# Performance work log

Measured on AMD Instinct MI355X. Metric: run time of the kernel, lower is better.

Reference implementation:

```python
import jax, jax.numpy as jnp
import numpy as np

N, E, IN_DIM, OUT_DIM = 20000, 320000, 256, 128
EPS = 1e-5  # PyG LayerNorm default eps


def seg_sum(data, idx, n):
    return jax.ops.segment_sum(data, idx, num_segments=n)


def gcn_conv(x, src, dst, emask, W, b, n):
    # GCNConv(improved=True): add self-loops with weight 2, symmetric deg^-1/2 norm.
    # Masked (dropped) edges contribute weight 0 to both degree and aggregation.
    xW = x @ W                               # [n, C_out]
    w = emask.astype(x.dtype)                # [E]
    deg = seg_sum(w, dst, n) + 2.0           # in-degree + self-loop weight 2
    dinv = jax.lax.rsqrt(deg)                # deg >= 2 always
    norm = dinv[src] * w * dinv[dst]         # [E]
    out = seg_sum(xW[src] * norm[:, None], dst, n)
    out = out + (2.0 / deg)[:, None] * xW    # self-loop term: dinv_i * 2 * dinv_i
    return out + b


def graph_norm(x, w, b):
    # PyG LayerNorm(mode='graph'), batch=None: scalar mean/std over ALL entries,
    # then per-channel affine.
    xc = x - x.mean()
    std = jnp.sqrt(jnp.mean(xc * xc))
    return xc / (std + EPS) * w + b


def sag_pool(x, src, dst, emask, wrel, brel, wroot, n, k):
    # SAGPooling: score from GraphConv(in,1) = lin_rel(sum_{j->i} x_j) + lin_root(x_i).
    # lin_rel commutes with the sum, so project to scalar first (cheaper).
    w = emask.astype(x.dtype)
    s_rel = (x @ wrel)[:, 0]                                  # [n]
    score = seg_sum(s_rel[src] * w, dst, n) + brel[0] + (x @ wroot)[:, 0]
    topv, perm = jax.lax.top_k(score, k)                      # ratio=0.5 -> k nodes
    xk = x[perm] * jnp.tanh(topv)[:, None]                    # nonlinearity=tanh
    kept = jnp.zeros((n,), bool).at[perm].set(True)
    inv = jnp.zeros((n,), src.dtype).at[perm].set(jnp.arange(k, dtype=src.dtype))
    new_mask = emask & kept[src] & kept[dst]                  # filter_adj, fixed-size + mask
    return xk, inv[src], inv[dst], new_mask


def setup_inputs() -> dict:
    key = jax.random.key(0)
    ks = jax.random.split(key, 20)
    f = jnp.float32
    inp = {
        "x": jax.random.normal(ks[0], (N, IN_DIM), f),
        "edge_index": jax.random.randint(ks[1], (2, E), 0, N, dtype=jnp.int32),
        "W1": jax.random.normal(ks[2], (IN_DIM, 512), f) * (1.0 / np.sqrt(IN_DIM)),
        "b1": jnp.zeros((512,), f),
        "ln1_w": jnp.ones((512,), f),
        "ln1_b": jnp.zeros((512,), f),
        "p1_wrel": jax.random.normal(ks[3], (512, 1), f) * (1.0 / np.sqrt(512)),
        "p1_brel": jnp.zeros((1,), f),
        "p1_wroot": jax.random.normal(ks[4], (512, 1), f) * (1.0 / np.sqrt(512)),
        "W2": jax.random.normal(ks[5], (512, 256), f) * (1.0 / np.sqrt(512)),
        "b2": jnp.zeros((256,), f),
        "ln2_w": jnp.ones((256,), f),
        "ln2_b": jnp.zeros((256,), f),
        "p2_wrel": jax.random.normal(ks[6], (256, 1), f) * (1.0 / np.sqrt(256)),
        "p2_brel": jnp.zeros((1,), f),
        "p2_wroot": jax.random.normal(ks[7], (256, 1), f) * (1.0 / np.sqrt(256)),
        "Wf": jax.random.normal(ks[8], (256, OUT_DIM), f) * (1.0 / np.sqrt(256)),
        "bf": jnp.zeros((OUT_DIM,), f),
    }
    return inp


def reference(x, edge_index, W1, b1, ln1_w, ln1_b, p1_wrel, p1_brel, p1_wroot,
              W2, b2, ln2_w, ln2_b, p2_wrel, p2_brel, p2_wroot, Wf, bf):
    src, dst = edge_index[0], edge_index[1]
    emask = jnp.ones((E,), bool)
    k1 = (N + 1) // 2   # ceil(0.5 * N)
    k2 = (k1 + 1) // 2

    h = gcn_conv(x, src, dst, emask, W1, b1, N)
    h = jax.nn.relu(graph_norm(h, ln1_w, ln1_b))
    h, src, dst, emask = sag_pool(h, src, dst, emask, p1_wrel, p1_brel, p1_wroot, N, k1)

    h = gcn_conv(h, src, dst, emask, W2, b2, k1)
    h = jax.nn.relu(graph_norm(h, ln2_w, ln2_b))
    h, src, dst, emask = sag_pool(h, src, dst, emask, p2_wrel, p2_brel, p2_wroot, k1, k2)

    g = h.mean(axis=0, keepdims=True)   # global_mean_pool, batch=None -> [1, 256]
    return g @ Wf + bf
```

## Files before the change

kernel.cpp:

```cpp
#include <hip/hip_runtime.h>
#include <math.h>

#define N1 20000
#define NE 320000
#define CIN 256
#define C1 512
#define C2 256
#define K1 10000
#define K2 5000
#define NOUT 128
#define EPSV 1e-5f
#define CM_ROWS 128

typedef __attribute__((ext_vector_type(8))) short bf16x8;
typedef __attribute__((ext_vector_type(4))) float f32x4;

static inline unsigned cdiv(unsigned a, unsigned b) { return (a + b - 1) / b; }

__device__ inline ushort f2bf(float f) {
    unsigned u = __float_as_uint(f);
    unsigned r = u + 0x7FFFu + ((u >> 16) & 1u);
    return (ushort)(r >> 16);
}
__device__ inline float bf2f(ushort u) { return __uint_as_float(((unsigned)u) << 16); }

__global__ void fill_i32(int* __restrict__ p, int v, int n) {
    int i = blockIdx.x * blockDim.x + threadIdx.x;
    if (i < n) p[i] = v;
}

__global__ void f32_to_bf16(const float* __restrict__ in, ushort* __restrict__ out, int n4) {
    int i = blockIdx.x * blockDim.x + threadIdx.x;
    if (i >= n4) return;
    float4 v = reinterpret_cast<const float4*>(in)[i];
    ushort4 o;
    o.x = f2bf(v.x); o.y = f2bf(v.y); o.z = f2bf(v.z); o.w = f2bf(v.w);
    reinterpret_cast<ushort4*>(out)[i] = o;
}

__global__ void conv_transpose_bf16(const float* __restrict__ W, ushort* __restrict__ Wt,
                                    int K, int N) {
    int i = blockIdx.x * blockDim.x + threadIdx.x;
    if (i >= K * N) return;
    int k = i / N, n = i % N;
    Wt[(size_t)n * K + k] = f2bf(W[i]);
}

template <bool BF16OUT, bool STATS>
__global__ __launch_bounds__(256)
void gemm_bf16_mfma(const ushort* __restrict__ A, const ushort* __restrict__ Bt,
                    const float* __restrict__ bias, float* __restrict__ C,
                    ushort* __restrict__ Cb, float* __restrict__ Sp, int M, int N, int K) {
    constexpr int BM = 128, BN = 128, BK = 32;
    constexpr int LDK = BK + 8;
    __shared__ ushort As[BM * LDK];
    __shared__ ushort Bs[BN * LDK];
    int tid = threadIdx.x;
    int wid = tid >> 6, lane = tid & 63;
    int wr = wid >> 1, wc = wid & 1;
    int bm = blockIdx.x * BM, bn = blockIdx.y * BN;
    int lg = lane >> 4, lm = lane & 15;
    f32x4 zero = {0.f, 0.f, 0.f, 0.f};
    f32x4 acc[4][4];
#pragma unroll
    for (int m = 0; m < 4; ++m)
#pragma unroll
        for (int n = 0; n < 4; ++n) acc[m][n] = zero;

    for (int k0 = 0; k0 < K; k0 += BK) {
#pragma unroll
        for (int it = 0; it < 2; ++it) {
            int task = tid * 2 + it;
            int row = task >> 2, c8 = (task & 3) * 8;
            int gm = bm + row;
            bf16x8 v = {0, 0, 0, 0, 0, 0, 0, 0};
            if (gm < M) v = *(const bf16x8*)&A[(size_t)gm * K + k0 + c8];
            *(bf16x8*)&As[row * LDK + c8] = v;
            int gn = bn + row;
            bf16x8 w = {0, 0, 0, 0, 0, 0, 0, 0};
            if (gn < N) w = *(const bf16x8*)&Bt[(size_t)gn * K + k0 + c8];
            *(bf16x8*)&Bs[row * LDK + c8] = w;
        }
        __syncthreads();
        bf16x8 af[4], bfr[4];
#pragma unroll
        for (int m = 0; m < 4; ++m)
            af[m] = *(bf16x8*)&As[(wr * 64 + m * 16 + lm) * LDK + lg * 8];
#pragma unroll
        for (int n = 0; n < 4; ++n)
            bfr[n] = *(bf16x8*)&Bs[(wc * 64 + n * 16 + lm) * LDK + lg * 8];
#pragma unroll
        for (int m = 0; m < 4; ++m)
#pragma unroll
            for (int n = 0; n < 4; ++n)
                acc[m][n] = __builtin_amdgcn_mfma_f32_16x16x32_bf16(af[m], bfr[n], acc[m][n], 0, 0, 0);
        __syncthreads();
    }
    float ls = 0.f, lq = 0.f;
#pragma unroll
    for (int m = 0; m < 4; ++m) {
#pragma unroll
        for (int n = 0; n < 4; ++n) {
            int col = bn + wc * 64 + n * 16 + lm;
            float bv = bias ? bias[col] : 0.f;
#pragma unroll
            for (int r = 0; r < 4; ++r) {
                int row = bm + wr * 64 + m * 16 + lg * 4 + r;
                if (row < M) {
                    float val = acc[m][n][r] + bv;
                    if (BF16OUT) Cb[(size_t)row * N + col] = f2bf(val);
                    else         C[(size_t)row * N + col] = val;
                    if (STATS) { ls += val; lq += val * val; }
                }
            }
        }
    }
    if (STATS) {
        __shared__ float rs[256], rq[256];
        rs[tid] = ls; rq[tid] = lq;
        __syncthreads();
        for (int off = 128; off > 0; off >>= 1) {
            if (tid < off) { rs[tid] += rs[tid + off]; rq[tid] += rq[tid + off]; }
            __syncthreads();
        }
        if (tid == 0) {
            int b = blockIdx.y * gridDim.x + blockIdx.x;
            Sp[2 * b] = rs[0];
            Sp[2 * b + 1] = rq[0];
        }
    }
}

__global__ void count_deg(const int* __restrict__ dst, const int* __restrict__ mask, int E,
                          int* __restrict__ cnt) {
    int e = blockIdx.x * blockDim.x + threadIdx.x;
    if (e >= E) return;
    if (mask && !mask[e]) return;
    atomicAdd(&cnt[dst[e]], 1);
}

__global__ void dp_partial(const int* __restrict__ cnt, int n, int* __restrict__ part) {
    int base = blockIdx.x * 1024 + (int)threadIdx.x * 4;
    int s = 0;
#pragma unroll
    for (int t = 0; t < 4; ++t) {
        int i = base + t;
        if (i < n) s += cnt[i];
    }
    for (int off = 32; off > 0; off >>= 1) s += __shfl_down(s, off);
    __shared__ int sg[4];
    int wid = threadIdx.x >> 6;
    if ((threadIdx.x & 63) == 0) sg[wid] = s;
    __syncthreads();
    if (threadIdx.x == 0) part[blockIdx.x] = sg[0] + sg[1] + sg[2] + sg[3];
}

__global__ void scan64k(int nb, int* __restrict__ part, int* __restrict__ row_n) {
    int lane = threadIdx.x;
    int v0 = (lane < nb) ? part[lane] : 0;
    int v = v0;
    for (int off = 1; off < 64; off <<= 1) {
        int vv = __shfl_up(v, off);
        if (lane >= off) v += vv;
    }
    if (lane == nb - 1) row_n[0] = v;
    if (lane < nb) part[lane] = v - v0;
}

__global__ void dp_final(const int* __restrict__ cnt, int n, const int* __restrict__ part,
                         int* __restrict__ rowstart, int* __restrict__ cursor,
                         float* __restrict__ deg, float* __restrict__ dinv) {
    int base = blockIdx.x * 1024 + (int)threadIdx.x * 4;
    int c[4];
    int s = 0;
#pragma unroll
    for (int t = 0; t < 4; ++t) {
        int i = base + t;
        c[t] = (i < n) ? cnt[i] : 0;
        s += c[t];
    }
    int lane = threadIdx.x & 63, wid = threadIdx.x >> 6;
    int si = s;
    for (int off = 1; off < 64; off <<= 1) {
        int vv = __shfl_up(si, off);
        if (lane >= off) si += vv;
    }
    __shared__ int wg[4];
    if (lane == 63) wg[wid] = si;
    __syncthreads();
    int woff = 0;
    for (int w = 0; w < wid; ++w) woff += wg[w];
    int excl = part[blockIdx.x] + (si - s) + woff;
#pragma unroll
    for (int t = 0; t < 4; ++t) {
        int i = base + t;
        if (i < n) {
            rowstart[i] = excl;
            cursor[i] = excl;
            float dg = (float)c[t] + 2.0f;
            deg[i] = dg;
            dinv[i] = rsqrtf(dg);
        }
        excl += c[t];
    }
}

__global__ void csr_scatter(const int* __restrict__ src, const int* __restrict__ dst,
                            const int* __restrict__ mask, int E,
                            int* __restrict__ cursor, int* __restrict__ csr_src) {
    int e = blockIdx.x * blockDim.x + threadIdx.x;
    if (e >= E) return;
    if (mask && !mask[e]) return;
    int pos = atomicAdd(&cursor[dst[e]], 1);
    csr_src[pos] = src[e];
}

__global__ void aggregate_xb(const int* __restrict__ rowstart, const int* __restrict__ csr_src,
                             const float* __restrict__ deg, const float* __restrict__ dinv,
                             const ushort* __restrict__ xb, ushort* __restrict__ out, int n) {
    int node = blockIdx.x * (blockDim.x >> 6) + ((int)threadIdx.x >> 6);
    if (node >= n) return;
    int lane = threadIdx.x & 63;
    int beg = rowstart[node], end = rowstart[node + 1];
    float di = dinv[node];
    float4 acc = make_float4(0.f, 0.f, 0.f, 0.f);
    int j = beg;
    for (; j + 8 <= end; j += 8) {
        int s[8];
#pragma unroll
        for (int u = 0; u < 8; ++u) s[u] = csr_src[j + u];
        float c[8];
#pragma unroll
        for (int u = 0; u < 8; ++u) c[u] = dinv[s[u]] * di;
        ushort4 t[8];
#pragma unroll
        for (int u = 0; u < 8; ++u)
            t[u] = reinterpret_cast<const ushort4*>(&xb[(size_t)s[u] * CIN])[lane];
#pragma unroll
        for (int u = 0; u < 8; ++u) {
            acc.x += c[u] * bf2f(t[u].x);
            acc.y += c[u] * bf2f(t[u].y);
            acc.z += c[u] * bf2f(t[u].z);
            acc.w += c[u] * bf2f(t[u].w);
        }
    }
    for (; j < end; ++j) {
        int s = csr_src[j];
        float coef = dinv[s] * di;
        ushort4 t = reinterpret_cast<const ushort4*>(&xb[(size_t)s * CIN])[lane];
        acc.x += coef * bf2f(t.x);
        acc.y += coef * bf2f(t.y);
        acc.z += coef * bf2f(t.z);
        acc.w += coef * bf2f(t.w);
    }
    float self = 2.0f / deg[node];
    ushort4 t = reinterpret_cast<const ushort4*>(&xb[(size_t)node * CIN])[lane];
    acc.x += self * bf2f(t.x);
    acc.y += self * bf2f(t.y);
    acc.z += self * bf2f(t.z);
    acc.w += self * bf2f(t.w);
    ushort4 o;
    o.x = f2bf(acc.x); o.y = f2bf(acc.y); o.z = f2bf(acc.z); o.w = f2bf(acc.w);
    reinterpret_cast<ushort4*>(&out[(size_t)node * CIN])[lane] = o;
}

__global__ void aggregate_csr_bf(const int* __restrict__ rowstart, const int* __restrict__ csr_src,
                                 const float* __restrict__ deg, const float* __restrict__ dinv,
                                 const ushort* __restrict__ xWb, const float* __restrict__ b,
                                 float* __restrict__ out, float* __restrict__ Sp, int n) {
    int node = blockIdx.x * (blockDim.x >> 6) + ((int)threadIdx.x >> 6);
    bool valid = node < n;
    int lane = threadIdx.x & 63;
    float ls = 0.f, lq = 0.f;
    if (valid) {
        int beg = rowstart[node], end = rowstart[node + 1];
        float di = dinv[node];
        float4 acc = make_float4(0.f, 0.f, 0.f, 0.f);
        int j = beg;
        for (; j + 8 <= end; j += 8) {
            int s[8];
#pragma unroll
            for (int u = 0; u < 8; ++u) s[u] = csr_src[j + u];
            float c[8];
#pragma unroll
            for (int u = 0; u < 8; ++u) c[u] = dinv[s[u]] * di;
            ushort4 t[8];
#pragma unroll
            for (int u = 0; u < 8; ++u)
                t[u] = reinterpret_cast<const ushort4*>(&xWb[(size_t)s[u] * C2])[lane];
#pragma unroll
            for (int u = 0; u < 8; ++u) {
                acc.x += c[u] * bf2f(t[u].x);
                acc.y += c[u] * bf2f(t[u].y);
                acc.z += c[u] * bf2f(t[u].z);
                acc.w += c[u] * bf2f(t[u].w);
            }
        }
        for (; j < end; ++j) {
            int s = csr_src[j];
            float coef = dinv[s] * di;
            ushort4 t = reinterpret_cast<const ushort4*>(&xWb[(size_t)s * C2])[lane];
            acc.x += coef * bf2f(t.x);
            acc.y += coef * bf2f(t.y);
            acc.z += coef * bf2f(t.z);
            acc.w += coef * bf2f(t.w);
        }
        float self = 2.0f / deg[node];
        ushort4 t = reinterpret_cast<const ushort4*>(&xWb[(size_t)node * C2])[lane];
        float4 bb = reinterpret_cast<const float4*>(b)[lane];
        float4 o;
        o.x = acc.x + self * bf2f(t.x) + bb.x;
        o.y = acc.y + self * bf2f(t.y) + bb.y;
        o.z = acc.z + self * bf2f(t.z) + bb.z;
        o.w = acc.w + self * bf2f(t.w) + bb.w;
        reinterpret_cast<float4*>(&out[(size_t)node * C2])[lane] = o;
        ls = o.x + o.y + o.z + o.w;
        lq = o.x * o.x + o.y * o.y + o.z * o.z + o.w * o.w;
    }
    __shared__ float rs[256], rq[256];
    rs[threadIdx.x] = ls; rq[threadIdx.x] = lq;
    __syncthreads();
    for (int off = 128; off > 0; off >>= 1) {
        if ((int)threadIdx.x < off) {
            rs[threadIdx.x] += rs[threadIdx.x + off];
            rq[threadIdx.x] += rq[threadIdx.x + off];
        }
        __syncthreads();
    }
    if (threadIdx.x == 0) {
        Sp[2 * blockIdx.x] = rs[0];
        Sp[2 * blockIdx.x + 1] = rq[0];
    }
}

__global__ void reduce_final(const float* __restrict__ Sp, int nb, float* __restrict__ S) {
    float s = 0.f, q = 0.f;
    for (int i = threadIdx.x; i < nb; i += 256) {
        s += Sp[2 * i];
        q += Sp[2 * i + 1];
    }
    __shared__ float ls[256], lq[256];
    ls[threadIdx.x] = s; lq[threadIdx.x] = q;
    __syncthreads();
    for (int off = 128; off > 0; off >>= 1) {
        if ((int)threadIdx.x < off) {
            ls[threadIdx.x] += ls[threadIdx.x + off];
            lq[threadIdx.x] += lq[threadIdx.x + off];
        }
        __syncthreads();
    }
    if (threadIdx.x == 0) { S[0] = ls[0]; S[1] = lq[0]; }
}

template <int C>
__global__ void norm_scores(const float* __restrict__ h, int n, const float* __restrict__ S,
                            float inv_cnt, const float* __restrict__ lnw,
                            const float* __restrict__ lnb, const float* __restrict__ wrel,
                            const float* __restrict__ brel, const float* __restrict__ wroot,
                            float* __restrict__ r, float* __restrict__ score) {
    int node = blockIdx.x * (blockDim.x >> 6) + ((int)threadIdx.x >> 6);
    if (node >= n) return;
    int lane = threadIdx.x & 63;
    float mean = S[0] * inv_cnt;
    float var = S[1] * inv_cnt - mean * mean;
    float istd = 1.f / (sqrtf(fmaxf(var, 0.f)) + EPSV);
    const float4* row = reinterpret_cast<const float4*>(&h[(size_t)node * C]);
    float sr = 0.f, st = 0.f;
#pragma unroll
    for (int kk = 0; kk < C / 256; ++kk) {
        int idx = lane + 64 * kk;
        float4 v = row[idx];
        float4 w = reinterpret_cast<const float4*>(lnw)[idx];
        float4 bb = reinterpret_cast<const float4*>(lnb)[idx];
        float4 w4 = reinterpret_cast<const float4*>(wrel)[idx];
        float4 o4 = reinterpret_cast<const float4*>(wroot)[idx];
        v.x = fmaxf((v.x - mean) * istd * w.x + bb.x, 0.f);
        v.y = fmaxf((v.y - mean) * istd * w.y + bb.y, 0.f);
        v.z = fmaxf((v.z - mean) * istd * w.z + bb.z, 0.f);
        v.w = fmaxf((v.w - mean) * istd * w.w + bb.w, 0.f);
        sr += v.x * w4.x + v.y * w4.y + v.z * w4.z + v.w * w4.w;
        st += v.x * o4.x + v.y * o4.y + v.z * o4.z + v.w * o4.w;
    }
    for (int off = 32; off > 0; off >>= 1) {
        sr += __shfl_down(sr, off);
        st += __shfl_down(st, off);
    }
    if (lane == 0) {
        r[node] = sr;
        score[node] = st + brel[0];
    }
}

__global__ void gather_score_key(const int* __restrict__ rowstart, const int* __restrict__ csr_src,
                                 const float* __restrict__ r, float* __restrict__ score,
                                 unsigned* __restrict__ key, int n) {
    int i = blockIdx.x * blockDim.x + threadIdx.x;
    if (i >= n) return;
    float s = score[i];
    int beg = rowstart[i], end = rowstart[i + 1];
    int j = beg;
    for (; j + 4 <= end; j += 4) {
        int s0 = csr_src[j], s1 = csr_src[j + 1], s2 = csr_src[j + 2], s3 = csr_src[j + 3];
        s += r[s0] + r[s1] + r[s2] + r[s3];
    }
    for (; j < end; ++j) s += r[csr_src[j]];
    score[i] = s;
    unsigned u = __float_as_uint(s);
    key[i] = (u & 0x80000000u) ? ~u : (u | 0x80000000u);
}

__global__ void select_thresh_reg(const unsigned* __restrict__ key, int n, unsigned k,
                                  unsigned* __restrict__ sel) {
    __shared__ unsigned hist[256];
    __shared__ unsigned wsum[16];
    __shared__ unsigned s_pref, s_rem;
    int t = threadIdx.x;
    int lane = t & 63, w = t >> 6;

    unsigned kv[20];
#pragma unroll
    for (int i = 0; i < 20; ++i) {
        int idx = t + 1024 * i;
        kv[i] = (idx < n) ? key[idx] : 0u;
    }

    if (t < 256) hist[t] = 0u;
    if (t == 0) { s_pref = 0u; s_rem = k; }
    __syncthreads();

    unsigned pref = 0u, msk = 0u, rem = k;
#pragma unroll
    for (int pass = 0; pass < 4; ++pass) {
        int shift = 24 - 8 * pass;
#pragma unroll
        for (int i = 0; i < 20; ++i) {
            int idx = t + 1024 * i;
            if (idx < n && (kv[i] & msk) == pref)
                atomicAdd(&hist[(kv[i] >> shift) & 255u], 1u);
        }
        __syncthreads();
        unsigned val = (t < 256) ? hist[255 - t] : 0u;
        unsigned si = val;
#pragma unroll
        for (int off = 1; off < 64; off <<= 1) {
            unsigned vv = __shfl_up(si, off);
            if (lane >= off) si += vv;
        }
        if (lane == 63 && w < 4) wsum[w] = si;
        __syncthreads();
        if (t < 256) hist[t] = 0u;
        if (t < 256) {
            unsigned wpre = 0u;
            for (int i = 0; i < w; ++i) wpre += wsum[i];
            unsigned incl = wpre + si;
            unsigned excl = incl - val;
            if (excl < rem && rem <= incl) {
                s_pref = pref | ((unsigned)(255 - t) << shift);
                s_rem = rem - excl;
            }
        }
        __syncthreads();
        pref = s_pref;
        rem = s_rem;
        msk = 0xFFFFFFFFu << shift;
    }
    if (t == 0) { sel[0] = pref; sel[1] = rem; }
}

__global__ void sc_partial(const unsigned* __restrict__ key, int n, const unsigned* __restrict__ sel,
                           int* __restrict__ gpart, int* __restrict__ epart) {
    unsigned thr = sel[0];
    int base = blockIdx.x * 1024 + (int)threadIdx.x * 4;
    int gs = 0, es = 0;
#pragma unroll
    for (int t = 0; t < 4; ++t) {
        int i = base + t;
        if (i < n) {
            unsigned u = key[i];
            gs += (u > thr); es += (u == thr);
        }
    }
    for (int off = 32; off > 0; off >>= 1) {
        gs += __shfl_down(gs, off);
        es += __shfl_down(es, off);
    }
    __shared__ int sg[4], se[4];
    int wid = threadIdx.x >> 6;
    if ((threadIdx.x & 63) == 0) { sg[wid] = gs; se[wid] = es; }
    __syncthreads();
    if (threadIdx.x == 0) {
        gpart[blockIdx.x] = sg[0] + sg[1] + sg[2] + sg[3];
        epart[blockIdx.x] = se[0] + se[1] + se[2] + se[3];
    }
}

__global__ void sc_final(const unsigned* __restrict__ key, int n, const unsigned* __restrict__ sel,
                         const int* __restrict__ gpart, const int* __restrict__ epart,
                         int* __restrict__ kept, int* __restrict__ inv) {
    unsigned thr = sel[0];
    int tie = (int)sel[1];
    int gp0 = 0, ep0 = 0;
    for (int b = 0; b < (int)blockIdx.x; ++b) { gp0 += gpart[b]; ep0 += epart[b]; }
    int base = blockIdx.x * 1024 + (int)threadIdx.x * 4;
    int gl[4], el[4];
    int gs = 0, es = 0;
#pragma unroll
    for (int t = 0; t < 4; ++t) {
        int i = base + t;
        gl[t] = 0; el[t] = 0;
        if (i < n) {
            unsigned u = key[i];
            gl[t] = (u > thr); el[t] = (u == thr);
        }
        gs += gl[t]; es += el[t];
    }
    int lane = threadIdx.x & 63, wid = threadIdx.x >> 6;
    int gi = gs, ei = es;
    for (int off = 1; off < 64; off <<= 1) {
        int gg = __shfl_up(gi, off), ee = __shfl_up(ei, off);
        if (lane >= off) { gi += gg; ei += ee; }
    }
    __shared__ int wg[4], we[4];
    if (lane == 63) { wg[wid] = gi; we[wid] = ei; }
    __syncthreads();
    int wgo = 0, weo = 0;
    for (int w = 0; w < wid; ++w) { wgo += wg[w]; weo += we[w]; }
    int gp = gp0 + (gi - gs) + wgo;
    int ep = ep0 + (ei - es) + weo;
#pragma unroll
    for (int t = 0; t < 4; ++t) {
        int i = base + t;
        if (i < n) {
            int keep = gl[t] | (el[t] & ((ep < tie) ? 1 : 0));
            kept[i] = keep;
            inv[i] = gp + ((ep < tie) ? ep : tie);
        }
        gp += gl[t]; ep += el[t];
    }
}

__global__ void pool_apply_rows(const float* __restrict__ h, const float* __restrict__ score,
                                const int* __restrict__ kept, const int* __restrict__ inv,
                                int n, const float* __restrict__ S, float inv_cnt,
                                const float* __restrict__ lnw, const float* __restrict__ lnb,
                                ushort* __restrict__ hp) {
    int node = blockIdx.x * (blockDim.x >> 6) + ((int)threadIdx.x >> 6);
    if (node >= n) return;
    if (!kept[node]) return;
    int lane = threadIdx.x & 63;
    float mean = S[0] * inv_cnt;
    float var = S[1] * inv_cnt - mean * mean;
    float istd = 1.f / (sqrtf(fmaxf(var, 0.f)) + EPSV);
    float tw = tanhf(score[node]);
    const float4* src = reinterpret_cast<const float4*>(&h[(size_t)node * C1]);
    ushort4* dst = reinterpret_cast<ushort4*>(&hp[(size_t)inv[node] * C1]);
#pragma unroll
    for (int v = 0; v < 2; ++v) {
        int idx = lane + 64 * v;
        float4 a = src[idx];
        float4 w = reinterpret_cast<const float4*>(lnw)[idx];
        float4 bb = reinterpret_cast<const float4*>(lnb)[idx];
        ushort4 o;
        o.x = f2bf(fmaxf((a.x - mean) * istd * w.x + bb.x, 0.f) * tw);
        o.y = f2bf(fmaxf((a.y - mean) * istd * w.y + bb.y, 0.f) * tw);
        o.z = f2bf(fmaxf((a.z - mean) * istd * w.z + bb.z, 0.f) * tw);
        o.w = f2bf(fmaxf((a.w - mean) * istd * w.w + bb.w, 0.f) * tw);
        dst[idx] = o;
    }
}

__global__ void edge_relabel(const int* __restrict__ src, const int* __restrict__ dst, int E,
                             const int* __restrict__ kept, const int* __restrict__ inv,
                             int* __restrict__ src2, int* __restrict__ dst2,
                             int* __restrict__ mask2) {
    int e = blockIdx.x * blockDim.x + threadIdx.x;
    if (e >= E) return;
    int s = src[e], d = dst[e];
    int m = kept[s] & kept[d];
    mask2[e] = m;
    src2[e] = m ? inv[s] : 0;
    dst2[e] = m ? inv[d] : 0;
}

__global__ void colmean_part(const float* __restrict__ h, const float* __restrict__ score,
                             const int* __restrict__ kept, int n, const float* __restrict__ S,
                             float inv_cnt, const float* __restrict__ lnw,
                             const float* __restrict__ lnb, float* __restrict__ Gp) {
    __shared__ float w[CM_ROWS];
    int i0 = blockIdx.x * CM_ROWS;
    int t = threadIdx.x;
    float mean = S[0] * inv_cnt;
    float var = S[1] * inv_cnt - mean * mean;
    float istd = 1.f / (sqrtf(fmaxf(var, 0.f)) + EPSV);
    float wn = lnw[t] * istd;
    float bn = lnb[t] - mean * wn;
    for (int i = t; i < CM_ROWS; i += 256) {
        int idx = i0 + i;
        w[i] = (idx < n && kept[idx]) ? tanhf(score[idx]) : 0.f;
    }
    __syncthreads();
    float acc = 0.f;
    int rows = min(CM_ROWS, n - i0);
#pragma unroll 8
    for (int ri = 0; ri < rows; ++ri)
        acc = fmaf(w[ri], fmaxf(fmaf(h[(size_t)(i0 + ri) * C2 + t], wn, bn), 0.f), acc);
    Gp[blockIdx.x * 256 + t] = acc;
}

__global__ void colmean_final(const float* __restrict__ Gp, int nb, float invk,
                              float* __restrict__ g) {
    int t = threadIdx.x;
    float s = 0.f;
    for (int b = 0; b < nb; ++b) s += Gp[b * 256 + t];
    g[t] = s * invk;
}

__global__ void final_gemv(const float* __restrict__ g, const float* __restrict__ Wf,
                           const float* __restrict__ bf, float* __restrict__ out) {
    int j = threadIdx.x;
    float s = bf[j];
    for (int c = 0; c < 256; ++c) s += g[c] * Wf[c * NOUT + j];
    out[j] = s;
}

extern "C" void kernel_launch(void* const* d_in, const int* in_sizes, int n_in,
                              void* d_out, int out_size, void* d_ws, size_t ws_size,
                              hipStream_t stream) {
    const float* x      = (const float*)d_in[0];
    const int*   ei     = (const int*)d_in[1];
    const float* W1     = (const float*)d_in[2];
    const float* b1     = (const float*)d_in[3];
    const float* ln1w   = (const float*)d_in[4];
    const float* ln1b   = (const float*)d_in[5];
    const float* p1wrel = (const float*)d_in[6];
    const float* p1brel = (const float*)d_in[7];
    const float* p1wroot= (const float*)d_in[8];
    const float* W2     = (const float*)d_in[9];
    const float* b2     = (const float*)d_in[10];
    const float* ln2w   = (const float*)d_in[11];
    const float* ln2b   = (const float*)d_in[12];
    const float* p2wrel = (const float*)d_in[13];
    const float* p2brel = (const float*)d_in[14];
    const float* p2wroot= (const float*)d_in[15];
    const float* Wf     = (const float*)d_in[16];
    const float* bf     = (const float*)d_in[17];
    float* out = (float*)d_out;
    char* ws = (char*)d_ws;

    const int* src1 = ei;
    const int* dst1 = ei + NE;

    const size_t o0     = 0;
    const size_t o1     = 40960000;
    const size_t oXb    = 51200000;
    const size_t oW1t   = 61440000;
    const size_t oW2t   = 61702144;
    const size_t oSrc2  = 61964288;
    const size_t oDst2  = 63244288;
    const size_t oMask2 = 64524288;
    const size_t oCsr   = 65804288;
    const size_t oRow   = 67084288;
    const size_t oCur   = 67164352;
    const size_t oDeg   = 67244352;
    const size_t oDinv  = 67324352;
    const size_t oR     = 67404352;
    const size_t oScore1= 67484352;
    const size_t oKeyu  = 67564352;
    const size_t oKept  = 67644352;
    const size_t oInv   = 67724352;
    const size_t oScore2= 67804352;
    const size_t oKeyu2 = 67844352;
    const size_t oKept2 = 67884352;
    const size_t oInv2  = 67924352;
    const size_t oS     = 67964352;
    const size_t oSel   = 67964416;
    const size_t oGpart = 67964480;
    const size_t oEpart = 67964736;
    const size_t oG     = 67964992;
    const size_t oGp    = 68232256;
    const size_t oSp    = 68314176;

    float*  h1    = (float*)(ws + o0);
    float*  h2    = (float*)(ws + o0);
    ushort* xW2b  = (ushort*)(ws + o0 + 10240000);
    ushort* aggb  = (ushort*)(ws + o1);
    ushort* h1pb  = (ushort*)(ws + o1);
    ushort* xb    = (ushort*)(ws + oXb);
    ushort* W1t   = (ushort*)(ws + oW1t);
    ushort* W2t   = (ushort*)(ws + oW2t);
    int*    src2  = (int*)(ws + oSrc2);
    int*    dst2  = (int*)(ws + oDst2);
    int*    mask2 = (int*)(ws + oMask2);
    int*    csr   = (int*)(ws + oCsr);
    int*    row   = (int*)(ws + oRow);
    int*    cur   = (int*)(ws + oCur);
    float*  deg   = (float*)(ws + oDeg);
    float*  dinv  = (float*)(ws + oDinv);
    float*  r     = (float*)(ws + oR);
    float*  score1= (float*)(ws + oScore1);
    unsigned* keyu  = (unsigned*)(ws + oKeyu);
    int*    kept  = (int*)(ws + oKept);
    int*    inv   = (int*)(ws + oInv);
    float*  score2= (float*)(ws + oScore2);
    unsigned* keyu2 = (unsigned*)(ws + oKeyu2);
    int*    kept2 = (int*)(ws + oKept2);
    int*    inv2  = (int*)(ws + oInv2);
    float*  S     = (float*)(ws + oS);
    unsigned* sel  = (unsigned*)(ws + oSel);
    int*    gpart = (int*)(ws + oGpart);
    int*    epart = (int*)(ws + oEpart);
    float*  g     = (float*)(ws + oG);
    float*  Gp    = (float*)(ws + oGp);
    float*  Sp    = (float*)(ws + oSp);

    const int nb1 = cdiv(N1, 1024);
    const int nb2 = cdiv(K1, 1024);
    const int nbc = cdiv(K1, CM_ROWS);
    const int g1x = cdiv(N1, 128), g1y = C1 / 128;
    const int agg2b = cdiv(K1, 4);

    f32_to_bf16<<<cdiv(N1 * CIN / 4, 256), 256, 0, stream>>>(x, xb, N1 * CIN / 4);

    fill_i32<<<cdiv(N1, 256), 256, 0, stream>>>(cur, 0, N1);
    count_deg<<<cdiv(NE, 256), 256, 0, stream>>>(dst1, nullptr, NE, cur);
    dp_partial<<<nb1, 256, 0, stream>>>(cur, N1, gpart);
    scan64k<<<1, 64, 0, stream>>>(nb1, gpart, row + N1);
    dp_final<<<nb1, 256, 0, stream>>>(cur, N1, gpart, row, cur, deg, dinv);
    csr_scatter<<<cdiv(NE, 256), 256, 0, stream>>>(src1, dst1, nullptr, NE, cur, csr);

    aggregate_xb<<<cdiv(N1, 4), 256, 0, stream>>>(row, csr, deg, dinv, xb, aggb, N1);

    conv_transpose_bf16<<<cdiv(CIN * C1, 256), 256, 0, stream>>>(W1, W1t, CIN, C1);
    gemm_bf16_mfma<false, true><<<dim3(g1x, g1y), 256, 0, stream>>>(
        aggb, W1t, b1, h1, nullptr, Sp, N1, C1, CIN);
    reduce_final<<<1, 256, 0, stream>>>(Sp, g1x * g1y, S);

    norm_scores<C1><<<cdiv(N1, 4), 256, 0, stream>>>(h1, N1, S, 1.f / ((float)N1 * C1),
                                                     ln1w, ln1b, p1wrel, p1brel, p1wroot, r, score1);
    gather_score_key<<<cdiv(N1, 256), 256, 0, stream>>>(row, csr, r, score1, keyu, N1);

    select_thresh_reg<<<1, 1024, 0, stream>>>(keyu, N1, K1, sel);
    sc_partial<<<nb1, 256, 0, stream>>>(keyu, N1, sel, gpart, epart);
    sc_final<<<nb1, 256, 0, stream>>>(keyu, N1, sel, gpart, epart, kept, inv);

    pool_apply_rows<<<cdiv(N1, 4), 256, 0, stream>>>(h1, score1, kept, inv, N1, S,
                                                     1.f / ((float)N1 * C1), ln1w, ln1b, h1pb);
    edge_relabel<<<cdiv(NE, 256), 256, 0, stream>>>(src1, dst1, NE, kept, inv, src2, dst2, mask2);

    conv_transpose_bf16<<<cdiv(C1 * C2, 256), 256, 0, stream>>>(W2, W2t, C1, C2);
    gemm_bf16_mfma<true, false><<<dim3(cdiv(K1, 128), C2 / 128), 256, 0, stream>>>(
        h1pb, W2t, nullptr, nullptr, xW2b, nullptr, K1, C2, C1);

    fill_i32<<<cdiv(K1, 256), 256, 0, stream>>>(cur, 0, K1);
    count_deg<<<cdiv(NE, 256), 256, 0, stream>>>(dst2, mask2, NE, cur);
    dp_partial<<<nb2, 256, 0, stream>>>(cur, K1, gpart);
    scan64k<<<1, 64, 0, stream>>>(nb2, gpart, row + K1);
    dp_final<<<nb2, 256, 0, stream>>>(cur, K1, gpart, row, cur, deg, dinv);
    csr_scatter<<<cdiv(NE, 256), 256, 0, stream>>>(src2, dst2, mask2, NE, cur, csr);

    aggregate_csr_bf<<<agg2b, 256, 0, stream>>>(row, csr, deg, dinv, xW2b, b2, h2, Sp, K1);
    reduce_final<<<1, 256, 0, stream>>>(Sp, agg2b, S);

    norm_scores<C2><<<cdiv(K1, 4), 256, 0, stream>>>(h2, K1, S, 1.f / ((float)K1 * C2),
                                                     ln2w, ln2b, p2wrel, p2brel, p2wroot, r, score2);
    gather_score_key<<<cdiv(K1, 256), 256, 0, stream>>>(row, csr, r, score2, keyu2, K1);

    select_thresh_reg<<<1, 1024, 0, stream>>>(keyu2, K1, K2, sel);
    sc_partial<<<nb2, 256, 0, stream>>>(keyu2, K1, sel, gpart, epart);
    sc_final<<<nb2, 256, 0, stream>>>(keyu2, K1, sel, gpart, epart, kept2, inv2);

    colmean_part<<<nbc, 256, 0, stream>>>(h2, score2, kept2, K1, S, 1.f / ((float)K1 * C2),
                                          ln2w, ln2b, Gp);
    colmean_final<<<1, 256, 0, stream>>>(Gp, nbc, 1.f / (float)K2, g);
    final_gemv<<<1, NOUT, 0, stream>>>(g, Wf, bf, out);
}
```

Baseline: 297.9 us.

## Collapse multi-kernel scans, top-k selection and reductions into fewer launches

```diff
diff --git a/kernel.cpp b/kernel.cpp
--- a/kernel.cpp
+++ b/kernel.cpp
@@ -11,6 +11,7 @@
 #define NOUT 128
 #define EPSV 1e-5f
 #define CM_ROWS 128
+#define KPT 20
 
 typedef __attribute__((ext_vector_type(8))) short bf16x8;
 typedef __attribute__((ext_vector_type(4))) float f32x4;
@@ -24,13 +25,29 @@
 }
 __device__ inline float bf2f(ushort u) { return __uint_as_float(((unsigned)u) << 16); }
 
-__global__ void fill_i32(int* __restrict__ p, int v, int n) {
+__device__ void block_stats(const float* __restrict__ Sp, int nb, float inv_cnt,
+                            float& mean, float& istd) {
+    __shared__ float bs_ls[256], bs_lq[256];
+    float s = 0.f, q = 0.f;
+    for (int i = threadIdx.x; i < nb; i += 256) { s += Sp[2 * i]; q += Sp[2 * i + 1]; }
+    bs_ls[threadIdx.x] = s; bs_lq[threadIdx.x] = q;
+    __syncthreads();
+    for (int off = 128; off > 0; off >>= 1) {
+        if ((int)threadIdx.x < off) {
+            bs_ls[threadIdx.x] += bs_ls[threadIdx.x + off];
+            bs_lq[threadIdx.x] += bs_lq[threadIdx.x + off];
+        }
+        __syncthreads();
+    }
+    mean = bs_ls[0] * inv_cnt;
+    float var = bs_lq[0] * inv_cnt - mean * mean;
+    istd = 1.f / (sqrtf(fmaxf(var, 0.f)) + EPSV);
+}
+
+__global__ void f32_to_bf16(const float* __restrict__ in, ushort* __restrict__ out, int n4,
+                            int* __restrict__ zbuf, int nz) {
     int i = blockIdx.x * blockDim.x + threadIdx.x;
-    if (i < n) p[i] = v;
-}
-
-__global__ void f32_to_bf16(const float* __restrict__ in, ushort* __restrict__ out, int n4) {
-    int i = blockIdx.x * blockDim.x + threadIdx.x;
+    if (i < nz) zbuf[i] = 0;
     if (i >= n4) return;
     float4 v = reinterpret_cast<const float4*>(in)[i];
     ushort4 o;
@@ -139,70 +156,46 @@
     atomicAdd(&cnt[dst[e]], 1);
 }
 
-__global__ void dp_partial(const int* __restrict__ cnt, int n, int* __restrict__ part) {
-    int base = blockIdx.x * 1024 + (int)threadIdx.x * 4;
+__global__ void scan_all(const int* __restrict__ cnt, int n, int* __restrict__ rowstart,
+                         int* __restrict__ cursor, float* __restrict__ deg,
+                         float* __restrict__ dinv) {
+    int t = threadIdx.x;
+    int lane = t & 63, w = t >> 6;
+    int base = t * KPT;
+    int c[KPT];
     int s = 0;
 #pragma unroll
-    for (int t = 0; t < 4; ++t) {
-        int i = base + t;
-        if (i < n) s += cnt[i];
-    }
-    for (int off = 32; off > 0; off >>= 1) s += __shfl_down(s, off);
-    __shared__ int sg[4];
-    int wid = threadIdx.x >> 6;
-    if ((threadIdx.x & 63) == 0) sg[wid] = s;
-    __syncthreads();
-    if (threadIdx.x == 0) part[blockIdx.x] = sg[0] + sg[1] + sg[2] + sg[3];
-}
-
-__global__ void scan64k(int nb, int* __restrict__ part, int* __restrict__ row_n) {
-    int lane = threadIdx.x;
-    int v0 = (lane < nb) ? part[lane] : 0;
-    int v = v0;
-    for (int off = 1; off < 64; off <<= 1) {
-        int vv = __shfl_up(v, off);
-        if (lane >= off) v += vv;
-    }
-    if (lane == nb - 1) row_n[0] = v;
-    if (lane < nb) part[lane] = v - v0;
-}
-
-__global__ void dp_final(const int* __restrict__ cnt, int n, const int* __restrict__ part,
-                         int* __restrict__ rowstart, int* __restrict__ cursor,
-                         float* __restrict__ deg, float* __restrict__ dinv) {
-    int base = blockIdx.x * 1024 + (int)threadIdx.x * 4;
-    int c[4];
-    int s = 0;
-#pragma unroll
-    for (int t = 0; t < 4; ++t) {
-        int i = base + t;
-        c[t] = (i < n) ? cnt[i] : 0;
-        s += c[t];
-    }
-    int lane = threadIdx.x & 63, wid = threadIdx.x >> 6;
+    for (int i = 0; i < KPT; ++i) {
+        int idx = base + i;
+        c[i] = (idx < n) ? cnt[idx] : 0;
+        s += c[i];
+    }
     int si = s;
     for (int off = 1; off < 64; off <<= 1) {
         int vv = __shfl_up(si, off);
         if (lane >= off) si += vv;
     }
-    __shared__ int wg[4];
-    if (lane == 63) wg[wid] = si;
+    __shared__ int wsum[16];
+    if (lane == 63) wsum[w] = si;
     __syncthreads();
-    int woff = 0;
-    for (int w = 0; w < wid; ++w) woff += wg[w];
-    int excl = part[blockIdx.x] + (si - s) + woff;
-#pragma unroll
-    for (int t = 0; t < 4; ++t) {
-        int i = base + t;
-        if (i < n) {
-            rowstart[i] = excl;
-            cursor[i] = excl;
-            float dg = (float)c[t] + 2.0f;
-            deg[i] = dg;
-            dinv[i] = rsqrtf(dg);
-        }
-        excl += c[t];
-    }
+    int wpre = 0;
+    for (int i = 0; i < w; ++i) wpre += wsum[i];
+    int total = 0;
+    for (int i = 0; i < 16; ++i) total += wsum[i];
+    int excl = wpre + si - s;
+#pragma unroll
+    for (int i = 0; i < KPT; ++i) {
+        int idx = base + i;
+        if (idx < n) {
+            rowstart[idx] = excl;
+            cursor[idx] = excl;
+            float dg = (float)c[i] + 2.0f;
+            deg[idx] = dg;
+            dinv[idx] = rsqrtf(dg);
+        }
+        excl += c[i];
+    }
+    if (t == 0) rowstart[n] = total;
 }
 
 __global__ void csr_scatter(const int* __restrict__ src, const int* __restrict__ dst,
@@ -333,37 +326,17 @@
     }
 }
 
-__global__ void reduce_final(const float* __restrict__ Sp, int nb, float* __restrict__ S) {
-    float s = 0.f, q = 0.f;
-    for (int i = threadIdx.x; i < nb; i += 256) {
-        s += Sp[2 * i];
-        q += Sp[2 * i + 1];
-    }
-    __shared__ float ls[256], lq[256];
-    ls[threadIdx.x] = s; lq[threadIdx.x] = q;
-    __syncthreads();
-    for (int off = 128; off > 0; off >>= 1) {
-        if ((int)threadIdx.x < off) {
-            ls[threadIdx.x] += ls[threadIdx.x + off];
-            lq[threadIdx.x] += lq[threadIdx.x + off];
-        }
-        __syncthreads();
-    }
-    if (threadIdx.x == 0) { S[0] = ls[0]; S[1] = lq[0]; }
-}
-
 template <int C>
-__global__ void norm_scores(const float* __restrict__ h, int n, const float* __restrict__ S,
-                            float inv_cnt, const float* __restrict__ lnw,
+__global__ void norm_scores(const float* __restrict__ h, int n, const float* __restrict__ Sp,
+                            int nb, float inv_cnt, const float* __restrict__ lnw,
                             const float* __restrict__ lnb, const float* __restrict__ wrel,
                             const float* __restrict__ brel, const float* __restrict__ wroot,
                             float* __restrict__ r, float* __restrict__ score) {
+    float mean, istd;
+    block_stats(Sp, nb, inv_cnt, mean, istd);
     int node = blockIdx.x * (blockDim.x >> 6) + ((int)threadIdx.x >> 6);
     if (node >= n) return;
     int lane = threadIdx.x & 63;
-    float mean = S[0] * inv_cnt;
-    float var = S[1] * inv_cnt - mean * mean;
-    float istd = 1.f / (sqrtf(fmaxf(var, 0.f)) + EPSV);
     const float4* row = reinterpret_cast<const float4*>(&h[(size_t)node * C]);
     float sr = 0.f, st = 0.f;
 #pragma unroll
@@ -409,46 +382,44 @@
     key[i] = (u & 0x80000000u) ? ~u : (u | 0x80000000u);
 }
 
-__global__ void select_thresh_reg(const unsigned* __restrict__ key, int n, unsigned k,
-                                  unsigned* __restrict__ sel) {
+__global__ void topk_all(const unsigned* __restrict__ key, int n, unsigned k,
+                         int* __restrict__ kept, int* __restrict__ inv) {
     __shared__ unsigned hist[256];
     __shared__ unsigned wsum[16];
     __shared__ unsigned s_pref, s_rem;
+    __shared__ int wgs[16], wes[16];
     int t = threadIdx.x;
     int lane = t & 63, w = t >> 6;
-
-    unsigned kv[20];
-#pragma unroll
-    for (int i = 0; i < 20; ++i) {
-        int idx = t + 1024 * i;
+    int base = t * KPT;
+
+    unsigned kv[KPT];
+#pragma unroll
+    for (int i = 0; i < KPT; ++i) {
+        int idx = base + i;
         kv[i] = (idx < n) ? key[idx] : 0u;
     }
-
     if (t < 256) hist[t] = 0u;
     if (t == 0) { s_pref = 0u; s_rem = k; }
     __syncthreads();
 
     unsigned pref = 0u, msk = 0u, rem = k;
-#pragma unroll
     for (int pass = 0; pass < 4; ++pass) {
         int shift = 24 - 8 * pass;
 #pragma unroll
-        for (int i = 0; i < 20; ++i) {
-            int idx = t + 1024 * i;
+        for (int i = 0; i < KPT; ++i) {
+            int idx = base + i;
             if (idx < n && (kv[i] & msk) == pref)
                 atomicAdd(&hist[(kv[i] >> shift) & 255u], 1u);
         }
         __syncthreads();
         unsigned val = (t < 256) ? hist[255 - t] : 0u;
         unsigned si = val;
-#pragma unroll
         for (int off = 1; off < 64; off <<= 1) {
             unsigned vv = __shfl_up(si, off);
             if (lane >= off) si += vv;
         }
         if (lane == 63 && w < 4) wsum[w] = si;
         __syncthreads();
-        if (t < 256) hist[t] = 0u;
         if (t < 256) {
             unsigned wpre = 0u;
             for (int i = 0; i < w; ++i) wpre += wsum[i];
@@ -459,98 +430,61 @@
                 s_rem = rem - excl;
             }
         }
+        if (t < 256) hist[t] = 0u;
         __syncthreads();
         pref = s_pref;
         rem = s_rem;
         msk = 0xFFFFFFFFu << shift;
     }
-    if (t == 0) { sel[0] = pref; sel[1] = rem; }
-}
-
-__global__ void sc_partial(const unsigned* __restrict__ key, int n, const unsigned* __restrict__ sel,
-                           int* __restrict__ gpart, int* __restrict__ epart) {
-    unsigned thr = sel[0];
-    int base = blockIdx.x * 1024 + (int)threadIdx.x * 4;
+    unsigned thr = pref;
+    int tie = (int)rem;
+
+    int gl[KPT], el[KPT];
     int gs = 0, es = 0;
 #pragma unroll
-    for (int t = 0; t < 4; ++t) {
-        int i = base + t;
-        if (i < n) {
-            unsigned u = key[i];
-            gs += (u > thr); es += (u == thr);
-        }
-    }
-    for (int off = 32; off > 0; off >>= 1) {
-        gs += __shfl_down(gs, off);
-        es += __shfl_down(es, off);
-    }
-    __shared__ int sg[4], se[4];
-    int wid = threadIdx.x >> 6;
-    if ((threadIdx.x & 63) == 0) { sg[wid] = gs; se[wid] = es; }
-    __syncthreads();
-    if (threadIdx.x == 0) {
-        gpart[blockIdx.x] = sg[0] + sg[1] + sg[2] + sg[3];
-        epart[blockIdx.x] = se[0] + se[1] + se[2] + se[3];
-    }
-}
-
-__global__ void sc_final(const unsigned* __restrict__ key, int n, const unsigned* __restrict__ sel,
-                         const int* __restrict__ gpart, const int* __restrict__ epart,
-                         int* __restrict__ kept, int* __restrict__ inv) {
-    unsigned thr = sel[0];
-    int tie = (int)sel[1];
-    int gp0 = 0, ep0 = 0;
-    for (int b = 0; b < (int)blockIdx.x; ++b) { gp0 += gpart[b]; ep0 += epart[b]; }
-    int base = blockIdx.x * 1024 + (int)threadIdx.x * 4;
-    int gl[4], el[4];
-    int gs = 0, es = 0;
-#pragma unroll
-    for (int t = 0; t < 4; ++t) {
-        int i = base + t;
-        gl[t] = 0; el[t] = 0;
-        if (i < n) {
-            unsigned u = key[i];
-            gl[t] = (u > thr); el[t] = (u == thr);
-        }
-        gs += gl[t]; es += el[t];
-    }
-    int lane = threadIdx.x & 63, wid = threadIdx.x >> 6;
+    for (int i = 0; i < KPT; ++i) {
+        int idx = base + i;
+        gl[i] = 0; el[i] = 0;
+        if (idx < n) {
+            gl[i] = (kv[i] > thr);
+            el[i] = (kv[i] == thr);
+        }
+        gs += gl[i]; es += el[i];
+    }
     int gi = gs, ei = es;
     for (int off = 1; off < 64; off <<= 1) {
         int gg = __shfl_up(gi, off), ee = __shfl_up(ei, off);
         if (lane >= off) { gi += gg; ei += ee; }
     }
-    __shared__ int wg[4], we[4];
-    if (lane == 63) { wg[wid] = gi; we[wid] = ei; }
+    if (lane == 63) { wgs[w] = gi; wes[w] = ei; }
     __syncthreads();
-    int wgo = 0, weo = 0;
-    for (int w = 0; w < wid; ++w) { wgo += wg[w]; weo += we[w]; }
-    int gp = gp0 + (gi - gs) + wgo;
-    int ep = ep0 + (ei - es) + weo;
-#pragma unroll
-    for (int t = 0; t < 4; ++t) {
-        int i = base + t;
-        if (i < n) {
-            int keep = gl[t] | (el[t] & ((ep < tie) ? 1 : 0));
-            kept[i] = keep;
-            inv[i] = gp + ((ep < tie) ? ep : tie);
-        }
-        gp += gl[t]; ep += el[t];
+    int gw = 0, ew = 0;
+    for (int i = 0; i < w; ++i) { gw += wgs[i]; ew += wes[i]; }
+    int gp = gw + gi - gs;
+    int ep = ew + ei - es;
+#pragma unroll
+    for (int i = 0; i < KPT; ++i) {
+        int idx = base + i;
+        if (idx < n) {
+            int keep = gl[i] | (el[i] & ((ep < tie) ? 1 : 0));
+            kept[idx] = keep;
+            inv[idx] = gp + ((ep < tie) ? ep : tie);
+        }
+        gp += gl[i]; ep += el[i];
     }
 }
 
 __global__ void pool_apply_rows(const float* __restrict__ h, const float* __restrict__ score,
                                 const int* __restrict__ kept, const int* __restrict__ inv,
-                                int n, const float* __restrict__ S, float inv_cnt,
+                                int n, const float* __restrict__ Sp, int nb, float inv_cnt,
                                 const float* __restrict__ lnw, const float* __restrict__ lnb,
                                 ushort* __restrict__ hp) {
+    float mean, istd;
+    block_stats(Sp, nb, inv_cnt, mean, istd);
     int node = blockIdx.x * (blockDim.x >> 6) + ((int)threadIdx.x >> 6);
     if (node >= n) return;
     if (!kept[node]) return;
     int lane = threadIdx.x & 63;
-    float mean = S[0] * inv_cnt;
-    float var = S[1] * inv_cnt - mean * mean;
-    float istd = 1.f / (sqrtf(fmaxf(var, 0.f)) + EPSV);
     float tw = tanhf(score[node]);
     const float4* src = reinterpret_cast<const float4*>(&h[(size_t)node * C1]);
     ushort4* dst = reinterpret_cast<ushort4*>(&hp[(size_t)inv[node] * C1]);
@@ -572,8 +506,9 @@
 __global__ void edge_relabel(const int* __restrict__ src, const int* __restrict__ dst, int E,
                              const int* __restrict__ kept, const int* __restrict__ inv,
                              int* __restrict__ src2, int* __restrict__ dst2,
-                             int* __restrict__ mask2) {
+                             int* __restrict__ mask2, int* __restrict__ zbuf, int nz) {
     int e = blockIdx.x * blockDim.x + threadIdx.x;
+    if (e < nz) zbuf[e] = 0;
     if (e >= E) return;
     int s = src[e], d = dst[e];
     int m = kept[s] & kept[d];
@@ -583,15 +518,14 @@
 }
 
 __global__ void colmean_part(const float* __restrict__ h, const float* __restrict__ score,
-                             const int* __restrict__ kept, int n, const float* __restrict__ S,
-                             float inv_cnt, const float* __restrict__ lnw,
+                             const int* __restrict__ kept, int n, const float* __restrict__ Sp,
+                             int nb, float inv_cnt, const float* __restrict__ lnw,
                              const float* __restrict__ lnb, float* __restrict__ Gp) {
+    float mean, istd;
+    block_stats(Sp, nb, inv_cnt, mean, istd);
     __shared__ float w[CM_ROWS];
     int i0 = blockIdx.x * CM_ROWS;
     int t = threadIdx.x;
-    float mean = S[0] * inv_cnt;
-    float var = S[1] * inv_cnt - mean * mean;
-    float istd = 1.f / (sqrtf(fmaxf(var, 0.f)) + EPSV);
     float wn = lnw[t] * istd;
     float bn = lnb[t] - mean * wn;
     for (int i = t; i < CM_ROWS; i += 256) {
@@ -607,20 +541,20 @@
     Gp[blockIdx.x * 256 + t] = acc;
 }
 
-__global__ void colmean_final(const float* __restrict__ Gp, int nb, float invk,
-                              float* __restrict__ g) {
+__global__ void final_fused(const float* __restrict__ Gp, int nb, float invk,
+                            const float* __restrict__ Wf, const float* __restrict__ bf,
+                            float* __restrict__ out) {
+    __shared__ float g[256];
     int t = threadIdx.x;
     float s = 0.f;
     for (int b = 0; b < nb; ++b) s += Gp[b * 256 + t];
     g[t] = s * invk;
-}
-
-__global__ void final_gemv(const float* __restrict__ g, const float* __restrict__ Wf,
-                           const float* __restrict__ bf, float* __restrict__ out) {
-    int j = threadIdx.x;
-    float s = bf[j];
-    for (int c = 0; c < 256; ++c) s += g[c] * Wf[c * NOUT + j];
-    out[j] = s;
+    __syncthreads();
+    if (t < NOUT) {
+        float acc = bf[t];
+        for (int c = 0; c < 256; ++c) acc = fmaf(g[c], Wf[c * NOUT + t], acc);
+        out[t] = acc;
+    }
 }
 
 extern "C" void kernel_launch(void* const* d_in, const int* in_sizes, int n_in,
@@ -672,11 +606,6 @@
     const size_t oKeyu2 = 67844352;
     const size_t oKept2 = 67884352;
     const size_t oInv2  = 67924352;
-    const size_t oS     = 67964352;
-    const size_t oSel   = 67964416;
-    const size_t oGpart = 67964480;
-    const size_t oEpart = 67964736;
-    const size_t oG     = 67964992;
     const size_t oGp    = 68232256;
     const size_t oSp    = 68314176;
 
@@ -705,27 +634,18 @@
     unsigned* keyu2 = (unsigned*)(ws + oKeyu2);
     int*    kept2 = (int*)(ws + oKept2);
     int*    inv2  = (int*)(ws + oInv2);
-    float*  S     = (float*)(ws + oS);
-    unsigned* sel  = (unsigned*)(ws + oSel);
-    int*    gpart = (int*)(ws + oGpart);
-    int*    epart = (int*)(ws + oEpart);
-    float*  g     = (float*)(ws + oG);
     float*  Gp    = (float*)(ws + oGp);
     float*  Sp    = (float*)(ws + oSp);
 
-    const int nb1 = cdiv(N1, 1024);
-    const int nb2 = cdiv(K1, 1024);
     const int nbc = cdiv(K1, CM_ROWS);
     const int g1x = cdiv(N1, 128), g1y = C1 / 128;
     const int agg2b = cdiv(K1, 4);
-
-    f32_to_bf16<<<cdiv(N1 * CIN / 4, 256), 256, 0, stream>>>(x, xb, N1 * CIN / 4);
-
-    fill_i32<<<cdiv(N1, 256), 256, 0, stream>>>(cur, 0, N1);
+    const float ic1 = 1.f / ((float)N1 * C1);
+    const float ic2 = 1.f / ((float)K1 * C2);
+
+    f32_to_bf16<<<cdiv(N1 * CIN / 4, 256), 256, 0, stream>>>(x, xb, N1 * CIN / 4, cur, N1);
     count_deg<<<cdiv(NE, 256), 256, 0, stream>>>(dst1, nullptr, NE, cur);
-    dp_partial<<<nb1, 256, 0, stream>>>(cur, N1, gpart);
-    scan64k<<<1, 64, 0, stream>>>(nb1, gpart, row + N1);
-    dp_final<<<nb1, 256, 0, stream>>>(cur, N1, gpart, row, cur, deg, dinv);
+    scan_all<<<1, 1024, 0, stream>>>(cur, N1, row, cur, deg, dinv);
     csr_scatter<<<cdiv(NE, 256), 256, 0, stream>>>(src1, dst1, nullptr, NE, cur, csr);
 
     aggregate_xb<<<cdiv(N1, 4), 256, 0, stream>>>(row, csr, deg, dinv, xb, aggb, N1);
@@ -733,44 +653,33 @@
     conv_transpose_bf16<<<cdiv(CIN * C1, 256), 256, 0, stream>>>(W1, W1t, CIN, C1);
     gemm_bf16_mfma<false, true><<<dim3(g1x, g1y), 256, 0, stream>>>(
         aggb, W1t, b1, h1, nullptr, Sp, N1, C1, CIN);
-    reduce_final<<<1, 256, 0, stream>>>(Sp, g1x * g1y, S);
-
-    norm_scores<C1><<<cdiv(N1, 4), 256, 0, stream>>>(h1, N1, S, 1.f / ((float)N1 * C1),
+
+    norm_scores<C1><<<cdiv(N1, 4), 256, 0, stream>>>(h1, N1, Sp, g1x * g1y, ic1,
                                                      ln1w, ln1b, p1wrel, p1brel, p1wroot, r, score1);
     gather_score_key<<<cdiv(N1, 256), 256, 0, stream>>>(row, csr, r, score1, keyu, N1);
-
-    select_thresh_reg<<<1, 1024, 0, stream>>>(keyu, N1, K1, sel);
-    sc_partial<<<nb1, 256, 0, stream>>>(keyu, N1, sel, gpart, epart);
-    sc_final<<<nb1, 256, 0, stream>>>(keyu, N1, sel, gpart, epart, kept, inv);
-
-    pool_apply_rows<<<cdiv(N1, 4), 256, 0, stream>>>(h1, score1, kept, inv, N1, S,
-                                                     1.f / ((float)N1 * C1), ln1w, ln1b, h1pb);
-    edge_relabel<<<cdiv(NE, 256), 256, 0, stream>>>(src1, dst1, NE, kept, inv, src2, dst2, mask2);
+    topk_all<<<1, 1024, 0, stream>>>(keyu, N1, K1, kept, inv);
+
+    pool_apply_rows<<<cdiv(N1, 4), 256, 0, stream>>>(h1, score1, kept, inv, N1, Sp, g1x * g1y,
+                                                     ic1, ln1w, ln1b, h1pb);
+    edge_relabel<<<cdiv(NE, 256), 256, 0, stream>>>(src1, dst1, NE, kept, inv,
+                                                    src2, dst2, mask2, cur, K1);
 
     conv_transpose_bf16<<<cdiv(C1 * C2, 256), 256, 0, stream>>>(W2, W2t, C1, C2);
     gemm_bf16_mfma<true, false><<<dim3(cdiv(K1, 128), C2 / 128), 256, 0, stream>>>(
         h1pb, W2t, nullptr, nullptr, xW2b, nullptr, K1, C2, C1);
 
-    fill_i32<<<cdiv(K1, 256), 256, 0, stream>>>(cur, 0, K1);
     count_deg<<<cdiv(NE, 256), 256, 0, stream>>>(dst2, mask2, NE, cur);
-    dp_partial<<<nb2, 256, 0, stream>>>(cur, K1, gpart);
-    scan64k<<<1, 64, 0, stream>>>(nb2, gpart, row + K1);
-    dp_final<<<nb2, 256, 0, stream>>>(cur, K1, gpart, row, cur, deg, dinv);
+    scan_all<<<1, 1024, 0, stream>>>(cur, K1, row, cur, deg, dinv);
     csr_scatter<<<cdiv(NE, 256), 256, 0, stream>>>(src2, dst2, mask2, NE, cur, csr);
 
     aggregate_csr_bf<<<agg2b, 256, 0, stream>>>(row, csr, deg, dinv, xW2b, b2, h2, Sp, K1);
-    reduce_final<<<1, 256, 0, stream>>>(Sp, agg2b, S);
-
-    norm_scores<C2><<<cdiv(K1, 4), 256, 0, stream>>>(h2, K1, S, 1.f / ((float)K1 * C2),
+
+    norm_scores<C2><<<cdiv(K1, 4), 256, 0, stream>>>(h2, K1, Sp, agg2b, ic2,
                                                      ln2w, ln2b, p2wrel, p2brel, p2wroot, r, score2);
     gather_score_key<<<cdiv(K1, 256), 256, 0, stream>>>(row, csr, r, score2, keyu2, K1);
-
-    select_thresh_reg<<<1, 1024, 0, stream>>>(keyu2, K1, K2, sel);
-    sc_partial<<<nb2, 256, 0, stream>>>(keyu2, K1, sel, gpart, epart);
-    sc_final<<<nb2, 256, 0, stream>>>(keyu2, K1, sel, gpart, epart, kept2, inv2);
-
-    colmean_part<<<nbc, 256, 0, stream>>>(h2, score2, kept2, K1, S, 1.f / ((float)K1 * C2),
+    topk_all<<<1, 1024, 0, stream>>>(keyu2, K1, K2, kept2, inv2);
+
+    colmean_part<<<nbc, 256, 0, stream>>>(h2, score2, kept2, K1, Sp, agg2b, ic2,
                                           ln2w, ln2b, Gp);
-    colmean_final<<<1, 256, 0, stream>>>(Gp, nbc, 1.f / (float)K2, g);
-    final_gemv<<<1, NOUT, 0, stream>>>(g, Wf, bf, out);
-}
+    final_fused<<<1, 256, 0, stream>>>(Gp, nbc, 1.f / (float)K2, Wf, bf, out);
+}
```

Measured after the change: 369.8 us. +24.1%, slower.
